# Kernel optimization log

Measured on AMD Instinct MI355X. Metric: run time of the kernel, lower is better.

Reference implementation:

```python
import jax, jax.numpy as jnp
import numpy as np

GROUPS = 32
K = 5          # up_kernel_size
UP = 2         # up_factor
EPS = 1e-5


def group_norm(x, w, b):
    B, C, H, W = x.shape
    xr = x.reshape(B, GROUPS, -1)
    mu = xr.mean(axis=2, keepdims=True)
    var = xr.var(axis=2, keepdims=True)
    xr = (xr - mu) * jax.lax.rsqrt(var + EPS)
    return xr.reshape(B, C, H, W) * w[None, :, None, None] + b[None, :, None, None]


def setup_inputs() -> dict:
    key = jax.random.key(0)
    ks = jax.random.split(key, 4)
    B, Cy, Cx, E, H, W = 4, 256, 256, 32, 64, 64
    return {
        "y": jax.random.normal(ks[0], (B, Cy, H * UP, W * UP), jnp.float32),
        "x": jax.random.normal(ks[1], (B, Cx, H, W), jnp.float32),
        "gn_y_w": jnp.ones((Cy,), jnp.float32),
        "gn_y_b": jnp.zeros((Cy,), jnp.float32),
        "gn_x_w": jnp.ones((Cx,), jnp.float32),
        "gn_x_b": jnp.zeros((Cx,), jnp.float32),
        "q_w": jax.random.normal(ks[2], (E, Cy), jnp.float32) * 0.02,
        "q_b": jnp.zeros((E,), jnp.float32),
        "k_w": jax.random.normal(ks[3], (E, Cx), jnp.float32) * 0.02,
        "k_b": jnp.zeros((E,), jnp.float32),
    }


def reference(y, x, gn_y_w, gn_y_b, gn_x_w, gn_x_b, q_w, q_b, k_w, k_b):
    pad = K // 2
    yn = group_norm(y, gn_y_w, gn_y_b)
    xn = group_norm(x, gn_x_w, gn_x_b)
    # 1x1 convs
    q = jnp.einsum('bchw,ec->behw', yn, q_w) + q_b[None, :, None, None]  # [B,E,Hu,Wu]
    k = jnp.einsum('bchw,ec->behw', xn, k_w) + k_b[None, :, None, None]  # [B,E,H,W]
    B, E, H, W = k.shape
    C = x.shape[1]
    # view q as per-low-res-cell blocks of UPxUP high-res queries
    q_r = q.reshape(B, E, H, UP, W, UP)
    k_pad = jnp.pad(k, ((0, 0), (0, 0), (pad, pad), (pad, pad)))  # zero pad (out-of-range -> 0 logit)
    v_pad = jnp.pad(x, ((0, 0), (0, 0), (pad, pad), (pad, pad)))
    # qk: logits over the KxK window (loop over 25 fixed offsets, vectorized inside)
    logits = []
    for dy in range(K):
        for dx in range(K):
            ks = k_pad[:, :, dy:dy + H, dx:dx + W]            # [B,E,H,W]
            logits.append(jnp.einsum('behuwv,behw->bhuwv', q_r, ks))
    logits = jnp.stack(logits, axis=1)                        # [B,KK,H,u,W,u]
    attn = jax.nn.softmax(logits, axis=1)
    # av: weighted aggregation of v over the same window
    out = jnp.zeros((B, C, H, UP, W, UP), x.dtype)
    idx = 0
    for dy in range(K):
        for dx in range(K):
            vs = v_pad[:, :, dy:dy + H, dx:dx + W]            # [B,C,H,W]
            out = out + attn[:, idx][:, None] * vs[:, :, :, None, :, None]
            idx += 1
    return out.reshape(B, C, H * UP, W * UP)
```

## Files before the change

### kernel.cpp

```cpp
#include <hip/hip_runtime.h>

#define EPSV 1e-5f

__global__ __launch_bounds__(256) void stats_kernel(const float* __restrict__ y,
                                                    const float* __restrict__ x,
                                                    float* __restrict__ part) {
    int bid = blockIdx.x;
    const float* src = (bid < 1024) ? (y + (size_t)bid * 16384)
                                    : (x + (size_t)(bid - 1024) * 16384);
    const float4* p = (const float4*)src;
    float s = 0.f, ss = 0.f;
    #pragma unroll 8
    for (int i = threadIdx.x; i < 4096; i += 256) {
        float4 v = p[i];
        s  += v.x + v.y + v.z + v.w;
        ss += v.x*v.x + v.y*v.y + v.z*v.z + v.w*v.w;
    }
    for (int off = 32; off > 0; off >>= 1) {
        s  += __shfl_down(s, off);
        ss += __shfl_down(ss, off);
    }
    __shared__ float red[8];
    int wid = threadIdx.x >> 6, lane = threadIdx.x & 63;
    if (lane == 0) { red[wid*2] = s; red[wid*2+1] = ss; }
    __syncthreads();
    if (threadIdx.x == 0) {
        part[bid*2+0] = red[0] + red[2] + red[4] + red[6];
        part[bid*2+1] = red[1] + red[3] + red[5] + red[7];
    }
}

__global__ __launch_bounds__(64) void make_eff_kernel(const float* __restrict__ qw, const float* __restrict__ qb,
                                                      const float* __restrict__ gyw, const float* __restrict__ gyb,
                                                      const float* __restrict__ kw, const float* __restrict__ kb,
                                                      const float* __restrict__ gxw, const float* __restrict__ gxb,
                                                      const float* __restrict__ part,
                                                      float* __restrict__ WeffQ, float* __restrict__ beffQ,
                                                      float* __restrict__ WeffK, float* __restrict__ beffK) {
    int id = blockIdx.x;
    int isK = id >> 7, b = (id >> 5) & 3, e = id & 31;
    const float* w     = isK ? kw  : qw;
    const float* bias  = isK ? kb  : qb;
    const float* gamma = isK ? gxw : gyw;
    const float* beta  = isK ? gxb : gyb;
    float inv_n = isK ? (1.f/32768.f) : (1.f/131072.f);
    float* W  = isK ? WeffK : WeffQ;
    float* be = isK ? beffK : beffQ;
    float partial = 0.f;
    for (int c = threadIdx.x; c < 256; c += 64) {
        int g = c >> 3, grp = b*32 + g;
        float s = 0.f, ss = 0.f;
        if (isK) {
            #pragma unroll
            for (int k2 = 0; k2 < 2; ++k2) {
                s  += part[(1024 + grp*2 + k2)*2 + 0];
                ss += part[(1024 + grp*2 + k2)*2 + 1];
            }
        } else {
            #pragma unroll
            for (int k2 = 0; k2 < 8; ++k2) {
                s  += part[(grp*8 + k2)*2 + 0];
                ss += part[(grp*8 + k2)*2 + 1];
            }
        }
        float mu = s * inv_n;
        float rs = rsqrtf(fmaf(-mu, mu, ss * inv_n) + EPSV);
        float wc = w[e*256 + c];
        float weff = wc * gamma[c] * rs;
        W[((size_t)b*256 + c)*32 + e] = weff;
        partial += wc * beta[c] - weff * mu;
    }
    for (int off = 32; off > 0; off >>= 1) partial += __shfl_down(partial, off);
    if (threadIdx.x == 0) be[b*32 + e] = partial + bias[e];
}

__global__ __launch_bounds__(256) void proj_kernel(const float* __restrict__ y, const float* __restrict__ x,
                                                   const float* __restrict__ WeffQ, const float* __restrict__ beffQ,
                                                   const float* __restrict__ WeffK, const float* __restrict__ beffK,
                                                   float* __restrict__ qbuf, float* __restrict__ kbuf) {
    int bid = blockIdx.x;
    int isX = bid >= 512;
    int lb = isX ? bid - 512 : bid;
    int b    = isX ? (lb >> 5) : (lb >> 7);
    int pxb  = isX ? (lb & 31) : (lb & 127);
    int npix = isX ? 4096 : 16384;
    const float* src   = isX ? x : y;
    const float* WeffT = isX ? WeffK : WeffQ;
    const float* beff  = isX ? beffK : beffQ;
    float* dst = isX ? kbuf : qbuf;

    int pix0 = pxb * 128 + (threadIdx.x & 63) * 2;
    int eg = __builtin_amdgcn_readfirstlane(threadIdx.x >> 6);
    const float* wp = WeffT + (size_t)b*256*32 + eg*8;
    float acc[2][8];
    #pragma unroll
    for (int j = 0; j < 8; ++j) {
        float bv = beff[b*32 + eg*8 + j];
        acc[0][j] = bv; acc[1][j] = bv;
    }
    const float* ysrc = src + (size_t)b*256*npix + pix0;
    #pragma unroll 8
    for (int c = 0; c < 256; ++c) {
        float2 t = *(const float2*)(ysrc + (size_t)c*npix);
        #pragma unroll
        for (int j = 0; j < 8; ++j) {
            float wj = wp[c*32 + j];
            acc[0][j] = fmaf(t.x, wj, acc[0][j]);
            acc[1][j] = fmaf(t.y, wj, acc[1][j]);
        }
    }
    float* dbase = dst + ((size_t)b*npix + pix0)*32 + eg*8;
    #pragma unroll
    for (int px = 0; px < 2; ++px) {
        float4 o0 = {acc[px][0], acc[px][1], acc[px][2], acc[px][3]};
        float4 o1 = {acc[px][4], acc[px][5], acc[px][6], acc[px][7]};
        *(float4*)(dbase + px*32 + 0) = o0;
        *(float4*)(dbase + px*32 + 4) = o1;
    }
}

__global__ __launch_bounds__(256) void attn_weights_kernel(const float* __restrict__ q,
                                                           const float* __restrict__ kk,
                                                           float* __restrict__ g_attn)
{
    __shared__ __align__(16) float sK[5184];
    __shared__ __align__(16) float sA[6400];
    int h0 = blockIdx.y * 8, w0 = blockIdx.x * 8;
    int b = blockIdx.z;
    int tid = threadIdx.x;

    for (int i = tid; i < 1152; i += 256) {
        int pos = i >> 3, e4 = i & 7;
        int r = pos / 12, c = pos - 12*r;
        int gh = h0 + r - 2, gw = w0 + c - 2;
        float4 v = make_float4(0.f, 0.f, 0.f, 0.f);
        if (gh >= 0 && gh < 64 && gw >= 0 && gw < 64)
            v = *(const float4*)(kk + (((size_t)b*4096 + gh*64 + gw)*32 + e4*4));
        *(float4*)&sK[pos*36 + e4*4] = v;
    }

    int h = tid >> 5, u = (tid >> 4) & 1, w = (tid >> 1) & 7, v = tid & 1;

    float qv[32];
    {
        int hh = 2*(h0 + h) + u, ww = 2*(w0 + w) + v;
        const float4* qp = (const float4*)(q + (((size_t)b*16384 + hh*128 + ww)*32));
        #pragma unroll
        for (int i4 = 0; i4 < 8; ++i4) {
            float4 t = qp[i4];
            qv[i4*4+0]=t.x; qv[i4*4+1]=t.y; qv[i4*4+2]=t.z; qv[i4*4+3]=t.w;
        }
    }
    __syncthreads();

    float a[25];
    const float* kbase = &sK[(h*12 + w)*36];
    #pragma unroll
    for (int j = 0; j < 25; ++j) {
        int dy = j / 5, dx = j - 5*dy;
        const float4* kp = (const float4*)(kbase + (dy*12 + dx)*36);
        float acc = 0.f;
        #pragma unroll
        for (int e4 = 0; e4 < 8; ++e4) {
            float4 kv = kp[e4];
            acc = fmaf(qv[e4*4+0], kv.x, acc);
            acc = fmaf(qv[e4*4+1], kv.y, acc);
            acc = fmaf(qv[e4*4+2], kv.z, acc);
            acc = fmaf(qv[e4*4+3], kv.w, acc);
        }
        a[j] = acc;
    }
    {
        float m = -1e30f;
        #pragma unroll
        for (int j = 0; j < 25; ++j) m = fmaxf(m, a[j]);
        float s = 0.f;
        #pragma unroll
        for (int j = 0; j < 25; ++j) { a[j] = __expf(a[j] - m); s += a[j]; }
        float inv = 1.f / s;
        #pragma unroll
        for (int j = 0; j < 25; ++j) sA[tid*25 + j] = a[j] * inv;
    }
    __syncthreads();

    float4* gdst = (float4*)(g_attn + ((size_t)b*64 + blockIdx.y*8 + blockIdx.x)*6400);
    const float4* ssrc = (const float4*)sA;
    for (int i = tid; i < 1600; i += 256) gdst[i] = ssrc[i];
}

__global__ __launch_bounds__(256) void gather_kernel(const float* __restrict__ g_attn,
                                                     const float* __restrict__ x,
                                                     float* __restrict__ out)
{
    __shared__ __align__(16) float sAttn[6400];
    __shared__ __align__(16) float sX[2880];
    int h0 = blockIdx.y * 8, w0 = blockIdx.x * 8;
    int b = blockIdx.z >> 2, slab = blockIdx.z & 3;
    int tid = threadIdx.x;

    {
        const float4* gsrc = (const float4*)(g_attn + ((size_t)b*64 + blockIdx.y*8 + blockIdx.x)*6400);
        float4* sdst = (float4*)sAttn;
        for (int i = tid; i < 1600; i += 256) sdst[i] = gsrc[i];
    }
    __syncthreads();

    float a[25];
    #pragma unroll
    for (int j = 0; j < 25; ++j) a[j] = sAttn[tid*25 + j];

    int h = tid >> 5, u = (tid >> 4) & 1, w = (tid >> 1) & 7, v = tid & 1;
    int hh = 2*(h0 + h) + u, ww = 2*(w0 + w) + v;
    int vbase = (h*12 + w)*20;

    for (int c0 = 0; c0 < 64; c0 += 16) {
        if (c0) __syncthreads();
        for (int i = 0; i < 9; ++i) {
            int t = i*256 + tid;
            int cc = t / 144, pos = t - 144*cc;
            int r = pos / 12, cl = pos - 12*r;
            int gh = h0 + r - 2, gw = w0 + cl - 2;
            float val = 0.f;
            if (gh >= 0 && gh < 64 && gw >= 0 && gw < 64)
                val = x[(((size_t)b*256 + slab*64 + c0 + cc)*64 + gh)*64 + gw];
            sX[pos*20 + cc] = val;
        }
        __syncthreads();

        #pragma unroll
        for (int g = 0; g < 4; ++g) {
            float o0 = 0.f, o1 = 0.f, o2 = 0.f, o3 = 0.f;
            const float* xb = &sX[vbase + g*4];
            #pragma unroll
            for (int j = 0; j < 25; ++j) {
                int dy = j / 5, dx = j - 5*dy;
                float4 xv = *(const float4*)(xb + (dy*12 + dx)*20);
                float aw = a[j];
                o0 = fmaf(aw, xv.x, o0);
                o1 = fmaf(aw, xv.y, o1);
                o2 = fmaf(aw, xv.z, o2);
                o3 = fmaf(aw, xv.w, o3);
            }
            size_t ob = (((size_t)b*256 + slab*64 + c0 + g*4)*128 + hh)*128 + ww;
            out[ob]           = o0;
            out[ob + 16384]   = o1;
            out[ob + 32768]   = o2;
            out[ob + 49152]   = o3;
        }
    }
}

extern "C" void kernel_launch(void* const* d_in, const int* in_sizes, int n_in,
                              void* d_out, int out_size, void* d_ws, size_t ws_size,
                              hipStream_t stream) {
    const float* y   = (const float*)d_in[0];
    const float* x   = (const float*)d_in[1];
    const float* gyw = (const float*)d_in[2];
    const float* gyb = (const float*)d_in[3];
    const float* gxw = (const float*)d_in[4];
    const float* gxb = (const float*)d_in[5];
    const float* qw  = (const float*)d_in[6];
    const float* qb  = (const float*)d_in[7];
    const float* kw  = (const float*)d_in[8];
    const float* kb  = (const float*)d_in[9];
    float* out = (float*)d_out;
    float* ws  = (float*)d_ws;

    float* part   = ws;
    float* WeffQ  = ws + 2560;
    float* beffQ  = ws + 35328;
    float* WeffK  = ws + 35456;
    float* beffK  = ws + 68224;
    float* qbuf   = ws + 68352;
    float* kbuf   = ws + 2165504;
    float* attnbf = ws + 2689792;

    stats_kernel<<<1280, 256, 0, stream>>>(y, x, part);
    make_eff_kernel<<<256, 64, 0, stream>>>(qw, qb, gyw, gyb, kw, kb, gxw, gxb,
                                            part, WeffQ, beffQ, WeffK, beffK);
    proj_kernel<<<640, 256, 0, stream>>>(y, x, WeffQ, beffQ, WeffK, beffK, qbuf, kbuf);
    attn_weights_kernel<<<dim3(8, 8, 4), 256, 0, stream>>>(qbuf, kbuf, attnbf);
    gather_kernel<<<dim3(8, 8, 16), 256, 0, stream>>>(attnbf, x, out);
}
```

Before: 210.6 us.

## Remap gather threads to cover 2x2 subpixels and share each loaded x value

The gather kernel's thread mapping is changed so each thread handles all four upsampled subpixels of one low-res cell for four channels. Each float4 read of x from shared memory is now reused across four attention weight sets, which cuts LDS traffic per FMA by four. Output stores become float2 pairs instead of scalar writes. In exchange each thread holds 100 attention weights and 16 accumulators in registers, which can lower occupancy or cause spills. The first-iteration barrier is also made unconditional.

Result: slower. 218.1 us (+3.6%).

```diff
diff --git a/kernel.cpp b/kernel.cpp
--- a/kernel.cpp
+++ b/kernel.cpp
@@ -205,16 +205,30 @@
     }
     __syncthreads();
 
-    float a[25];
+    int W    = tid >> 6;
+    int lane = tid & 63;
+    int cg   = lane >> 4;
+    int hp   = (lane >> 3) & 1;
+    int w    = lane & 7;
+    int h    = W*2 + hp;
+
+    float a4[4][25];
     #pragma unroll
-    for (int j = 0; j < 25; ++j) a[j] = sAttn[tid*25 + j];
-
-    int h = tid >> 5, u = (tid >> 4) & 1, w = (tid >> 1) & 7, v = tid & 1;
-    int hh = 2*(h0 + h) + u, ww = 2*(w0 + w) + v;
-    int vbase = (h*12 + w)*20;
+    for (int u = 0; u < 2; ++u) {
+        #pragma unroll
+        for (int v = 0; v < 2; ++v) {
+            const float* ap = &sAttn[(32*h + 16*u + 2*w + v)*25];
+            #pragma unroll
+            for (int j = 0; j < 25; ++j) a4[u*2+v][j] = ap[j];
+        }
+    }
+
+    int vbase = (h*12 + w)*20 + cg*4;
+    int hh0 = 2*(h0 + h);
+    int ww  = 2*(w0 + w);
 
     for (int c0 = 0; c0 < 64; c0 += 16) {
-        if (c0) __syncthreads();
+        __syncthreads();
         for (int i = 0; i < 9; ++i) {
             int t = i*256 + tid;
             int cc = t / 144, pos = t - 144*cc;
@@ -227,25 +241,34 @@
         }
         __syncthreads();
 
-        #pragma unroll
-        for (int g = 0; g < 4; ++g) {
-            float o0 = 0.f, o1 = 0.f, o2 = 0.f, o3 = 0.f;
-            const float* xb = &sX[vbase + g*4];
-            #pragma unroll
-            for (int j = 0; j < 25; ++j) {
-                int dy = j / 5, dx = j - 5*dy;
-                float4 xv = *(const float4*)(xb + (dy*12 + dx)*20);
-                float aw = a[j];
-                o0 = fmaf(aw, xv.x, o0);
-                o1 = fmaf(aw, xv.y, o1);
-                o2 = fmaf(aw, xv.z, o2);
-                o3 = fmaf(aw, xv.w, o3);
+        float acc[4][4];
+        #pragma unroll
+        for (int ci = 0; ci < 4; ++ci)
+            #pragma unroll
+            for (int c = 0; c < 4; ++c) acc[ci][c] = 0.f;
+
+        #pragma unroll
+        for (int j = 0; j < 25; ++j) {
+            int dy = j / 5, dx = j - 5*dy;
+            float4 xv = *(const float4*)&sX[vbase + (dy*12 + dx)*20];
+            #pragma unroll
+            for (int c = 0; c < 4; ++c) {
+                float aw = a4[c][j];
+                acc[0][c] = fmaf(aw, xv.x, acc[0][c]);
+                acc[1][c] = fmaf(aw, xv.y, acc[1][c]);
+                acc[2][c] = fmaf(aw, xv.z, acc[2][c]);
+                acc[3][c] = fmaf(aw, xv.w, acc[3][c]);
             }
-            size_t ob = (((size_t)b*256 + slab*64 + c0 + g*4)*128 + hh)*128 + ww;
-            out[ob]           = o0;
-            out[ob + 16384]   = o1;
-            out[ob + 32768]   = o2;
-            out[ob + 49152]   = o3;
+        }
+
+        #pragma unroll
+        for (int ci = 0; ci < 4; ++ci) {
+            int ch = slab*64 + c0 + cg*4 + ci;
+            #pragma unroll
+            for (int u = 0; u < 2; ++u) {
+                float2 o = make_float2(acc[ci][u*2+0], acc[ci][u*2+1]);
+                *(float2*)&out[(((size_t)b*256 + ch)*128 + (hh0 + u))*128 + ww] = o;
+            }
         }
     }
 }
```
